# Kernel optimization log

Hardware: AMD Instinct MI355X
Metric: run time of the kernel (lower is better)

Reference implementation:

```python
import jax, jax.numpy as jnp
import numpy as np

N = 131072
C = 8
W = 256


def setup_inputs() -> dict:
    key = jax.random.key(0)
    ks = jax.random.split(key, 10)
    s1 = 1.0 / np.sqrt(3.0)
    sw = 1.0 / np.sqrt(W)
    return {
        "positions": jax.random.normal(ks[0], (N, 3), dtype=jnp.float32),
        "times": jax.random.randint(ks[1], (N,), 0, C, dtype=jnp.int64),
        "W1": jax.random.normal(ks[2], (C, 3, W), dtype=jnp.float32) * s1,
        "b1": jnp.zeros((C, W), dtype=jnp.float32),
        "W2": jax.random.normal(ks[3], (C, W, W), dtype=jnp.float32) * sw,
        "b2": jnp.zeros((C, W), dtype=jnp.float32),
        "W3": jax.random.normal(ks[4], (C, W, W), dtype=jnp.float32) * sw,
        "b3": jnp.zeros((C, W), dtype=jnp.float32),
        "W4": jax.random.normal(ks[5], (C, W, 3), dtype=jnp.float32) * sw,
        "b4": jnp.zeros((C, 3), dtype=jnp.float32),
    }


def _mlp(x, w1, c1, w2, c2, w3, c3, w4, c4):
    # 4-layer MLP, Tanh hidden activations and Tanh output activation
    h = jnp.tanh(x @ w1 + c1)
    h = jnp.tanh(h @ w2 + c2)
    h = jnp.tanh(h @ w3 + c3)
    return jnp.tanh(h @ w4 + c4)


def reference(positions, times, W1, b1, W2, b2, W3, b3, W4, b4):
    # offsets = zeros_like(positions); offsets[times==i] = mlp_i(positions[times==i])
    # classes partition the points, so this equals a per-class select-sum.
    offsets = jnp.zeros_like(positions)
    for i in range(C):  # small fixed class count
        out_i = _mlp(positions, W1[i], b1[i], W2[i], b2[i], W3[i], b3[i], W4[i], b4[i])
        mask = (times == i)[:, None]  # [N,1]
        offsets = jnp.where(mask, out_i, offsets)
    return offsets
```

## Files before the change

kernel.cpp:

```cpp
#include <hip/hip_runtime.h>
#include <stdint.h>

#define N_PTS 131072
#define NCLS 8
#define HID 256
#define MT 128
#define CAP 32768

typedef __bf16 bf16x8 __attribute__((ext_vector_type(8)));
typedef float f32x4 __attribute__((ext_vector_type(4)));

__device__ __forceinline__ float tanh_p2(float a) {
  return fmaf(-2.0f, __builtin_amdgcn_rcpf(__expf(a) + 1.0f), 1.0f);
}

__device__ __forceinline__ unsigned short f2bf_rne(float f) {
  unsigned u = __float_as_uint(f);
  u = u + 0x7fffu + ((u >> 16) & 1u);
  return (unsigned short)(u >> 16);
}

__device__ __forceinline__ unsigned pack_bf16(float a, float b) {
  unsigned ua = __float_as_uint(a) + 0x8000u;
  unsigned ub = __float_as_uint(b) + 0x8000u;
  return __builtin_amdgcn_perm(ub, ua, 0x07060302u);
}

#define PK_TILES 256
#define MISC_BLKS 177
#define MISC_N 45184
#define SCAT_BLKS 128
#define PREP_GRID (PK_TILES + MISC_BLKS + SCAT_BLKS)

__global__ __launch_bounds__(256) void k_prep(
    const int* __restrict__ times,
    const float* __restrict__ W1, const float* __restrict__ b1,
    const float* __restrict__ W2, const float* __restrict__ b2,
    const float* __restrict__ W3, const float* __restrict__ b3,
    const float* __restrict__ W4, const float* __restrict__ b4,
    int* __restrict__ hdr, int* __restrict__ sortedIdx,
    unsigned short* __restrict__ packed23,
    float* __restrict__ w1p, float* __restrict__ b2p,
    float* __restrict__ b3p, float* __restrict__ b4p,
    unsigned short* __restrict__ W4p) {
  __shared__ unsigned short T[64][64];

  int b = blockIdx.x;
  int tid = threadIdx.x;

  if (b < PK_TILES) {
    int cl = b >> 4;
    int l = cl >> 3, c = cl & 7;
    int tile = b & 15;
    int k0 = (tile >> 2) * 64, j0 = (tile & 3) * 64;
    const float* W = (l ? W3 : W2) + c * 65536;
#pragma unroll
    for (int it = 0; it < 4; it++) {
      int f = tid + it * 256;
      int row = f >> 4, cg = f & 15;
      float4 v = *(const float4*)&W[(k0 + row) * 256 + j0 + cg * 4];
      T[row][cg * 4 + 0] = f2bf_rne(2.0f * v.x);
      T[row][cg * 4 + 1] = f2bf_rne(2.0f * v.y);
      T[row][cg * 4 + 2] = f2bf_rne(2.0f * v.z);
      T[row][cg * 4 + 3] = f2bf_rne(2.0f * v.w);
    }
    __syncthreads();
#pragma unroll
    for (int it = 0; it < 2; it++) {
      int g = tid + it * 256;
      int kb = g >> 6, j = g & 63;
      unsigned u[8];
#pragma unroll
      for (int uu = 0; uu < 8; uu++) u[uu] = T[kb * 8 + uu][j];
      uint4 pk = make_uint4(u[0] | (u[1] << 16), u[2] | (u[3] << 16),
                            u[4] | (u[5] << 16), u[6] | (u[7] << 16));
      int base = cl * 65536 + (((k0 >> 3) + kb) * 256 + (j0 + j)) * 8;
      *(uint4*)&packed23[base] = pk;
    }
  } else if (b < PK_TILES + MISC_BLKS) {
    int e2 = (b - PK_TILES) * 256 + tid;
    if (e2 < 8192) {
      int c = e2 >> 10, rem = e2 & 1023;
      int j = rem >> 2, t = rem & 3;
      float v = (t < 3) ? W1[c * 768 + t * 256 + j] : b1[c * 256 + j];
      w1p[e2] = 2.0f * v;
    } else if (e2 < 10240) {
      int i = e2 - 8192;
      b2p[i] = 2.0f * b2[i];
    } else if (e2 < 12288) {
      int i = e2 - 10240;
      b3p[i] = 2.0f * b3[i];
    } else if (e2 < 12416) {
      int i = e2 - 12288;
      int c = i >> 4, r = i & 15;
      b4p[i] = (r < 3) ? 2.0f * b4[c * 3 + r] : 0.0f;
    } else if (e2 < MISC_N) {
      int i = e2 - 12416;
      int c = i >> 12, rem = i & 4095;
      int jj = rem & 7, j = (rem >> 3) & 15, k = ((rem >> 7) << 3) + jj;
      float v = (j < 3) ? 2.0f * W4[c * 768 + k * 3 + j] : 0.0f;
      W4p[c * 4096 + rem] = f2bf_rne(v);
    }
  } else {
    __shared__ int gcnt[16][NCLS];
    __shared__ int gpre[16][NCLS];
    __shared__ int gbase[NCLS];
    int sb = b - (PK_TILES + MISC_BLKS);
    int lane = tid & 63, w = tid >> 6;
    int4 tv = ((const int4*)times)[sb * 256 + tid];
    int tcl[4] = {tv.x, tv.y, tv.z, tv.w};
    int rank[4];
#pragma unroll
    for (int s = 0; s < 4; s++) {
      int t = tcl[s];
      unsigned long long m0 = __ballot(t == 0), m1 = __ballot(t == 1);
      unsigned long long m2 = __ballot(t == 2), m3 = __ballot(t == 3);
      unsigned long long m4 = __ballot(t == 4), m5 = __ballot(t == 5);
      unsigned long long m6 = __ballot(t == 6), m7 = __ballot(t == 7);
      unsigned long long x0 = (t & 1) ? m1 : m0, x1 = (t & 1) ? m3 : m2;
      unsigned long long x2 = (t & 1) ? m5 : m4, x3 = (t & 1) ? m7 : m6;
      unsigned long long y0 = (t & 2) ? x1 : x0, y1 = (t & 2) ? x3 : x2;
      unsigned long long mo = (t & 4) ? y1 : y0;
      rank[s] = __popcll(mo & ((1ull << lane) - 1ull));
      if (lane == 0) {
        int g = w * 4 + s;
        gcnt[g][0] = __popcll(m0); gcnt[g][1] = __popcll(m1);
        gcnt[g][2] = __popcll(m2); gcnt[g][3] = __popcll(m3);
        gcnt[g][4] = __popcll(m4); gcnt[g][5] = __popcll(m5);
        gcnt[g][6] = __popcll(m6); gcnt[g][7] = __popcll(m7);
      }
    }
    __syncthreads();
    if (tid < NCLS) {
      int run = 0;
#pragma unroll
      for (int g = 0; g < 16; g++) { gpre[g][tid] = run; run += gcnt[g][tid]; }
      gbase[tid] = run ? atomicAdd(&hdr[tid], run) : 0;
    }
    __syncthreads();
    int i0 = (sb * 256 + tid) * 4;
#pragma unroll
    for (int s = 0; s < 4; s++) {
      int t = tcl[s];
      int g = w * 4 + s;
      sortedIdx[t * CAP + gbase[t] + gpre[g][t] + rank[s]] = i0 + s;
    }
  }
}

__device__ __forceinline__ void mfma_layer_T(
    unsigned short (*__restrict__ Abuf)[MT][8],
    const unsigned short* __restrict__ Apack,
    const float* __restrict__ biasp,
    int tid) {
  int lane = tid & 63, w = tid >> 6;
  int quad = lane >> 4, l16 = lane & 15;
  int jcol = w * 32 + l16;
  const bf16x8* __restrict__ Af = (const bf16x8*)Apack;

  f32x4 acc[2][8];
#pragma unroll
  for (int jf = 0; jf < 2; jf++) {
    f32x4 bv = *(const f32x4*)&biasp[w * 32 + jf * 16 + quad * 4];
#pragma unroll
    for (int mt = 0; mt < 8; mt++) acc[jf][mt] = bv;
  }

#pragma unroll
  for (int kb = 0; kb < 8; kb++) {
    int kq = kb * 4 + quad;
    bf16x8 af[2], bfr[8];
#pragma unroll
    for (int jf = 0; jf < 2; jf++) af[jf] = Af[kq * 256 + jcol + jf * 16];
#pragma unroll
    for (int mt = 0; mt < 8; mt++)
      bfr[mt] = *(const bf16x8*)&Abuf[kq][mt * 16 + l16][0];
#pragma unroll
    for (int jf = 0; jf < 2; jf++)
#pragma unroll
      for (int mt = 0; mt < 8; mt++)
        acc[jf][mt] = __builtin_amdgcn_mfma_f32_16x16x32_bf16(af[jf], bfr[mt], acc[jf][mt], 0, 0, 0);
  }

  __syncthreads();

#pragma unroll
  for (int jf = 0; jf < 2; jf++) {
    int jbase = w * 32 + jf * 16 + quad * 4;
#pragma unroll
    for (int mt = 0; mt < 8; mt++) {
      float t0 = tanh_p2(acc[jf][mt][0]);
      float t1 = tanh_p2(acc[jf][mt][1]);
      float t2 = tanh_p2(acc[jf][mt][2]);
      float t3 = tanh_p2(acc[jf][mt][3]);
      uint2 pk = make_uint2(pack_bf16(t0, t1), pack_bf16(t2, t3));
      *(uint2*)&Abuf[jbase >> 3][mt * 16 + l16][jbase & 7] = pk;
    }
  }
}

__global__ __launch_bounds__(512, 4) void k_mlp(
    const float* __restrict__ pos,
    const int* __restrict__ hdr, const int* __restrict__ sortedIdx,
    const unsigned short* __restrict__ packed23,
    const float* __restrict__ w1p, const float* __restrict__ b2p,
    const float* __restrict__ b3p, const float* __restrict__ b4p,
    const unsigned short* __restrict__ W4p,
    float* __restrict__ out) {

  __shared__ __align__(16) unsigned short Abuf[32][MT][8];
  __shared__ __align__(16) float4 w1i[256];
  __shared__ __align__(16) float4 xpos4[MT];
  __shared__ int sIdx[MT];

  int b = blockIdx.x;
  int tid = threadIdx.x;

  int c = -1, t0 = 0, cnt = 0;
  {
    int ts = 0;
#pragma unroll
    for (int cc = 0; cc < NCLS; cc++) {
      int cc_cnt = hdr[cc];
      int tiles = (cc_cnt + MT - 1) >> 7;
      if (b >= ts && b < ts + tiles) { c = cc; t0 = b - ts; cnt = cc_cnt; }
      ts += tiles;
    }
  }
  if (c < 0) return;
  int base = c * CAP + t0 * MT;
  int mCount = min(MT, cnt - t0 * MT);

  if (tid < MT) sIdx[tid] = sortedIdx[base + min(tid, mCount - 1)];
  if (tid < 256) w1i[tid] = ((const float4*)(w1p + (size_t)c * 1024))[tid];
  __syncthreads();
  if (tid < MT) {
    int idx = sIdx[tid] * 3;
    xpos4[tid] = make_float4(pos[idx], pos[idx + 1], pos[idx + 2], 0.0f);
  }
  __syncthreads();

  {
    int m = tid & (MT - 1), q = tid >> 7;
    float4 xp = xpos4[m];
#pragma unroll
    for (int i8 = 0; i8 < 8; i8++) {
      int j8 = q * 8 + i8;
      unsigned pk[4];
#pragma unroll
      for (int jp = 0; jp < 4; jp++) {
        float t[2];
#pragma unroll
        for (int u = 0; u < 2; u++) {
          float4 wv = w1i[j8 * 8 + jp * 2 + u];
          float a = fmaf(xp.x, wv.x, fmaf(xp.y, wv.y, fmaf(xp.z, wv.z, wv.w)));
          t[u] = tanh_p2(a);
        }
        pk[jp] = pack_bf16(t[0], t[1]);
      }
      *(uint4*)&Abuf[j8][m][0] = make_uint4(pk[0], pk[1], pk[2], pk[3]);
    }
  }
  __syncthreads();

  mfma_layer_T(Abuf, packed23 + ((size_t)c << 16), b2p + c * 256, tid);
  __syncthreads();
  mfma_layer_T(Abuf, packed23 + ((size_t)(8 + c) << 16), b3p + c * 256, tid);
  __syncthreads();

  {
    int lane = tid & 63, w = tid >> 6;
    int quad = lane >> 4, l16 = lane & 15;
    f32x4 acc = *(const f32x4*)&b4p[c * 16 + quad * 4];
#pragma unroll
    for (int kb = 0; kb < 8; kb++) {
      int kq = kb * 4 + quad;
      bf16x8 a4 = *(const bf16x8*)&W4p[((size_t)c * 512 + kq * 16 + l16) * 8];
      bf16x8 b4f = *(const bf16x8*)&Abuf[kq][w * 16 + l16][0];
      acc = __builtin_amdgcn_mfma_f32_16x16x32_bf16(a4, b4f, acc, 0, 0, 0);
    }
    int m = w * 16 + l16;
    if (quad == 0 && m < mCount) {
      int o = sIdx[m] * 3;
      out[o + 0] = tanh_p2(acc[0]);
      out[o + 1] = tanh_p2(acc[1]);
      out[o + 2] = tanh_p2(acc[2]);
    }
  }
}

extern "C" void kernel_launch(void* const* d_in, const int* in_sizes, int n_in,
                              void* d_out, int out_size, void* d_ws, size_t ws_size,
                              hipStream_t stream) {
  const float* pos = (const float*)d_in[0];
  const int* times = (const int*)d_in[1];
  const float* W1 = (const float*)d_in[2];
  const float* b1 = (const float*)d_in[3];
  const float* W2 = (const float*)d_in[4];
  const float* b2 = (const float*)d_in[5];
  const float* W3 = (const float*)d_in[6];
  const float* b3 = (const float*)d_in[7];
  const float* W4 = (const float*)d_in[8];
  const float* b4 = (const float*)d_in[9];

  char* ws = (char*)d_ws;
  int* hdr = (int*)ws;
  int* sortedIdx = (int*)(ws + 4096);
  float* w1p = (float*)(ws + 1052672);
  float* b2p = (float*)(ws + 1085440);
  float* b3p = (float*)(ws + 1093632);
  float* b4p = (float*)(ws + 1101824);
  unsigned short* W4p = (unsigned short*)(ws + 1102336);
  unsigned short* packed23 = (unsigned short*)(ws + (2u << 20));
  float* out = (float*)d_out;

  hipMemsetAsync(d_ws, 0, 64, stream);
  k_prep<<<PREP_GRID, 256, 0, stream>>>(times, W1, b1, W2, b2, W3, b3, W4, b4,
                                        hdr, sortedIdx, packed23,
                                        w1p, b2p, b3p, b4p, W4p);
  k_mlp<<<N_PTS / MT + NCLS, 512, 0, stream>>>(
      pos, hdr, sortedIdx, packed23, w1p, b2p, b3p, b4p, W4p, out);
}
```

Measured before the change: 137.5 us.

## Shrink MLP point tile to 32, raise occupancy, use exp2 with prescaled weights

Cuts the per-block point tile from 128 to 32, which shrinks the accumulator arrays and LDS footprint. The launch bound now requests 8 blocks per CU, and there are four times as many blocks. The tanh now uses a native exp2, with all weights and biases prescaled by 2/ln2 in the pack step. Layer-1 weights are read straight from global memory instead of being staged in LDS, and s_setprio is raised around the MFMA loops. The trade-off is that each block reloads the full layer-2/3 weights for fewer points, which increases weight traffic and lowers reuse per block.

```diff
diff --git a/kernel.cpp b/kernel.cpp
--- a/kernel.cpp
+++ b/kernel.cpp
@@ -4,14 +4,16 @@
 #define N_PTS 131072
 #define NCLS 8
 #define HID 256
-#define MT 128
+#define MT 32
 #define CAP 32768
+
+#define PSC 2.8853900817779268f
 
 typedef __bf16 bf16x8 __attribute__((ext_vector_type(8)));
 typedef float f32x4 __attribute__((ext_vector_type(4)));
 
 __device__ __forceinline__ float tanh_p2(float a) {
-  return fmaf(-2.0f, __builtin_amdgcn_rcpf(__expf(a) + 1.0f), 1.0f);
+  return fmaf(-2.0f, __builtin_amdgcn_rcpf(__builtin_amdgcn_exp2f(a) + 1.0f), 1.0f);
 }
 
 __device__ __forceinline__ unsigned short f2bf_rne(float f) {
@@ -59,10 +61,10 @@
       int f = tid + it * 256;
       int row = f >> 4, cg = f & 15;
       float4 v = *(const float4*)&W[(k0 + row) * 256 + j0 + cg * 4];
-      T[row][cg * 4 + 0] = f2bf_rne(2.0f * v.x);
-      T[row][cg * 4 + 1] = f2bf_rne(2.0f * v.y);
-      T[row][cg * 4 + 2] = f2bf_rne(2.0f * v.z);
-      T[row][cg * 4 + 3] = f2bf_rne(2.0f * v.w);
+      T[row][cg * 4 + 0] = f2bf_rne(PSC * v.x);
+      T[row][cg * 4 + 1] = f2bf_rne(PSC * v.y);
+      T[row][cg * 4 + 2] = f2bf_rne(PSC * v.z);
+      T[row][cg * 4 + 3] = f2bf_rne(PSC * v.w);
     }
     __syncthreads();
 #pragma unroll
@@ -83,22 +85,22 @@
       int c = e2 >> 10, rem = e2 & 1023;
       int j = rem >> 2, t = rem & 3;
       float v = (t < 3) ? W1[c * 768 + t * 256 + j] : b1[c * 256 + j];
-      w1p[e2] = 2.0f * v;
+      w1p[e2] = PSC * v;
     } else if (e2 < 10240) {
       int i = e2 - 8192;
-      b2p[i] = 2.0f * b2[i];
+      b2p[i] = PSC * b2[i];
     } else if (e2 < 12288) {
       int i = e2 - 10240;
-      b3p[i] = 2.0f * b3[i];
+      b3p[i] = PSC * b3[i];
     } else if (e2 < 12416) {
       int i = e2 - 12288;
       int c = i >> 4, r = i & 15;
-      b4p[i] = (r < 3) ? 2.0f * b4[c * 3 + r] : 0.0f;
+      b4p[i] = (r < 3) ? PSC * b4[c * 3 + r] : 0.0f;
     } else if (e2 < MISC_N) {
       int i = e2 - 12416;
       int c = i >> 12, rem = i & 4095;
       int jj = rem & 7, j = (rem >> 3) & 15, k = ((rem >> 7) << 3) + jj;
-      float v = (j < 3) ? 2.0f * W4[c * 768 + k * 3 + j] : 0.0f;
+      float v = (j < 3) ? PSC * W4[c * 768 + k * 3 + j] : 0.0f;
       W4p[c * 4096 + rem] = f2bf_rne(v);
     }
   } else {
@@ -158,29 +160,31 @@
   int jcol = w * 32 + l16;
   const bf16x8* __restrict__ Af = (const bf16x8*)Apack;
 
-  f32x4 acc[2][8];
+  f32x4 acc[2][2];
 #pragma unroll
   for (int jf = 0; jf < 2; jf++) {
     f32x4 bv = *(const f32x4*)&biasp[w * 32 + jf * 16 + quad * 4];
 #pragma unroll
-    for (int mt = 0; mt < 8; mt++) acc[jf][mt] = bv;
-  }
-
+    for (int mt = 0; mt < 2; mt++) acc[jf][mt] = bv;
+  }
+
+  __builtin_amdgcn_s_setprio(1);
 #pragma unroll
   for (int kb = 0; kb < 8; kb++) {
     int kq = kb * 4 + quad;
-    bf16x8 af[2], bfr[8];
+    bf16x8 af[2], bfr[2];
 #pragma unroll
     for (int jf = 0; jf < 2; jf++) af[jf] = Af[kq * 256 + jcol + jf * 16];
 #pragma unroll
-    for (int mt = 0; mt < 8; mt++)
+    for (int mt = 0; mt < 2; mt++)
       bfr[mt] = *(const bf16x8*)&Abuf[kq][mt * 16 + l16][0];
 #pragma unroll
     for (int jf = 0; jf < 2; jf++)
 #pragma unroll
-      for (int mt = 0; mt < 8; mt++)
+      for (int mt = 0; mt < 2; mt++)
         acc[jf][mt] = __builtin_amdgcn_mfma_f32_16x16x32_bf16(af[jf], bfr[mt], acc[jf][mt], 0, 0, 0);
   }
+  __builtin_amdgcn_s_setprio(0);
 
   __syncthreads();
 
@@ -188,7 +192,7 @@
   for (int jf = 0; jf < 2; jf++) {
     int jbase = w * 32 + jf * 16 + quad * 4;
 #pragma unroll
-    for (int mt = 0; mt < 8; mt++) {
+    for (int mt = 0; mt < 2; mt++) {
       float t0 = tanh_p2(acc[jf][mt][0]);
       float t1 = tanh_p2(acc[jf][mt][1]);
       float t2 = tanh_p2(acc[jf][mt][2]);
@@ -199,7 +203,7 @@
   }
 }
 
-__global__ __launch_bounds__(512, 4) void k_mlp(
+__global__ __launch_bounds__(512, 8) void k_mlp(
     const float* __restrict__ pos,
     const int* __restrict__ hdr, const int* __restrict__ sortedIdx,
     const unsigned short* __restrict__ packed23,
@@ -209,7 +213,6 @@
     float* __restrict__ out) {
 
   __shared__ __align__(16) unsigned short Abuf[32][MT][8];
-  __shared__ __align__(16) float4 w1i[256];
   __shared__ __align__(16) float4 xpos4[MT];
   __shared__ int sIdx[MT];
 
@@ -222,7 +225,7 @@
 #pragma unroll
     for (int cc = 0; cc < NCLS; cc++) {
       int cc_cnt = hdr[cc];
-      int tiles = (cc_cnt + MT - 1) >> 7;
+      int tiles = (cc_cnt + MT - 1) >> 5;
       if (b >= ts && b < ts + tiles) { c = cc; t0 = b - ts; cnt = cc_cnt; }
       ts += tiles;
     }
@@ -232,7 +235,6 @@
   int mCount = min(MT, cnt - t0 * MT);
 
   if (tid < MT) sIdx[tid] = sortedIdx[base + min(tid, mCount - 1)];
-  if (tid < 256) w1i[tid] = ((const float4*)(w1p + (size_t)c * 1024))[tid];
   __syncthreads();
   if (tid < MT) {
     int idx = sIdx[tid] * 3;
@@ -241,18 +243,19 @@
   __syncthreads();
 
   {
-    int m = tid & (MT - 1), q = tid >> 7;
+    const float4* __restrict__ w1g = (const float4*)(w1p + (size_t)c * 1024);
+    int m = tid & (MT - 1), q = tid >> 5;
     float4 xp = xpos4[m];
 #pragma unroll
-    for (int i8 = 0; i8 < 8; i8++) {
-      int j8 = q * 8 + i8;
+    for (int i8 = 0; i8 < 2; i8++) {
+      int j8 = q * 2 + i8;
       unsigned pk[4];
 #pragma unroll
       for (int jp = 0; jp < 4; jp++) {
         float t[2];
 #pragma unroll
         for (int u = 0; u < 2; u++) {
-          float4 wv = w1i[j8 * 8 + jp * 2 + u];
+          float4 wv = w1g[j8 * 8 + jp * 2 + u];
           float a = fmaf(xp.x, wv.x, fmaf(xp.y, wv.y, fmaf(xp.z, wv.z, wv.w)));
           t[u] = tanh_p2(a);
         }
@@ -270,21 +273,26 @@
 
   {
     int lane = tid & 63, w = tid >> 6;
-    int quad = lane >> 4, l16 = lane & 15;
-    f32x4 acc = *(const f32x4*)&b4p[c * 16 + quad * 4];
-#pragma unroll
-    for (int kb = 0; kb < 8; kb++) {
-      int kq = kb * 4 + quad;
-      bf16x8 a4 = *(const bf16x8*)&W4p[((size_t)c * 512 + kq * 16 + l16) * 8];
-      bf16x8 b4f = *(const bf16x8*)&Abuf[kq][w * 16 + l16][0];
-      acc = __builtin_amdgcn_mfma_f32_16x16x32_bf16(a4, b4f, acc, 0, 0, 0);
-    }
-    int m = w * 16 + l16;
-    if (quad == 0 && m < mCount) {
-      int o = sIdx[m] * 3;
-      out[o + 0] = tanh_p2(acc[0]);
-      out[o + 1] = tanh_p2(acc[1]);
-      out[o + 2] = tanh_p2(acc[2]);
+    if (w < 2) {
+      int quad = lane >> 4, l16 = lane & 15;
+      const bf16x8* __restrict__ W4f = (const bf16x8*)W4p;
+      f32x4 acc = *(const f32x4*)&b4p[c * 16 + quad * 4];
+      __builtin_amdgcn_s_setprio(1);
+#pragma unroll
+      for (int kb = 0; kb < 8; kb++) {
+        int kq = kb * 4 + quad;
+        bf16x8 a4 = W4f[(size_t)c * 512 + kq * 16 + l16];
+        bf16x8 b4f = *(const bf16x8*)&Abuf[kq][w * 16 + l16][0];
+        acc = __builtin_amdgcn_mfma_f32_16x16x32_bf16(a4, b4f, acc, 0, 0, 0);
+      }
+      __builtin_amdgcn_s_setprio(0);
+      int m = w * 16 + l16;
+      if (quad == 0 && m < mCount) {
+        int o = sIdx[m] * 3;
+        out[o + 0] = tanh_p2(acc[0]);
+        out[o + 1] = tanh_p2(acc[1]);
+        out[o + 2] = tanh_p2(acc[2]);
+      }
     }
   }
 }
```

After: 143.2 us. +4.1%, slower.
